# Optimization experiments

Hardware: AMD Instinct MI355X
Metric: run time of the kernel (lower is better)

## Reference

```python
import jax, jax.numpy as jnp
import numpy as np

TEMPERATURE = 0.5
EPS = 1e-8  # matches torch CosineSimilarity eps


def setup_inputs() -> dict:
    key = jax.random.key(0)
    k1, k2 = jax.random.split(key)
    N, D = 4096, 256
    z1 = jax.random.normal(k1, (N, D), dtype=jnp.float32)
    z2 = jax.random.normal(k2, (N, D), dtype=jnp.float32)
    return {"z1": z1, "z2": z2}


def reference(z1, z2):
    N = z1.shape[0]
    z = jnp.concatenate([z1, z2], axis=0)            # [2N, D]
    norm = jnp.linalg.norm(z, axis=-1, keepdims=True)
    zn = z / jnp.maximum(norm, EPS)                  # L2-normalized
    sim = (zn @ zn.T) / TEMPERATURE                  # [2N, 2N] cosine sim / temp
    # mask self-similarity on the diagonal
    diag = jnp.eye(2 * N, dtype=bool)
    sim = jnp.where(diag, -jnp.inf, sim)
    # positive pair labels: row i pairs with i+N (first half) or i-N (second half)
    labels = jnp.concatenate([jnp.arange(N) + N, jnp.arange(N)])
    logp = jax.nn.log_softmax(sim, axis=-1)
    loss = -jnp.mean(logp[jnp.arange(2 * N), labels])
    return loss
```

## Files before the change

kernel.cpp:

```cpp
#include <hip/hip_runtime.h>
#include <hip/hip_bf16.h>


#define NROWS 8192
#define NHALF 4096
#define DDIM  256

typedef __bf16 bf16;
typedef __bf16 bf16x4 __attribute__((ext_vector_type(4)));
typedef __bf16 bf16x8 __attribute__((ext_vector_type(8)));
typedef float  f32x4  __attribute__((ext_vector_type(4)));

__constant__ const float kTwoLog2e = 2.8853900817779268f;
__constant__ const float kLn2      = 0.6931471805599453f;

__device__ __forceinline__ const float* zrow(const float* z1, const float* z2, int r) {
  return (r < NHALF) ? (z1 + (size_t)r * DDIM) : (z2 + (size_t)(r - NHALF) * DDIM);
}

__global__ void k_normalize(const float* __restrict__ z1, const float* __restrict__ z2,
                            bf16* __restrict__ zn, float* __restrict__ invn,
                            float* __restrict__ rowsum, float* __restrict__ out) {
  const int wave = threadIdx.x >> 6, lane = threadIdx.x & 63;
  const int row = blockIdx.x * 4 + wave;
  const float* src = zrow(z1, z2, row);
  f32x4 v = *(const f32x4*)(src + lane * 4);
  float ss = v.x * v.x + v.y * v.y + v.z * v.z + v.w * v.w;
#pragma unroll
  for (int off = 1; off < 64; off <<= 1) ss += __shfl_xor(ss, off);
  const float inv = 1.0f / fmaxf(sqrtf(ss), 1e-8f);
  bf16x4 o;
  o.x = (bf16)(v.x * inv); o.y = (bf16)(v.y * inv);
  o.z = (bf16)(v.z * inv); o.w = (bf16)(v.w * inv);
  *(bf16x4*)(zn + (size_t)row * DDIM + lane * 4) = o;
  if (lane == 0) { invn[row] = inv; rowsum[row] = 0.0f; }
  if (blockIdx.x == 0 && threadIdx.x == 0) out[0] = 0.0f;
}

#define NBLK 512

typedef const __attribute__((address_space(1))) unsigned int* as1_u32p;
typedef __attribute__((address_space(3))) unsigned int* as3_u32p;

__device__ __forceinline__ void load_lds16(const void* g, void* l) {
  __builtin_amdgcn_global_lo\
ad_lds((as1_u32p)g, (as3_u32p)l, 16, 0, 0);
}

__global__ __launch_bounds__(256, 2) void k_gram(const bf16* __restrict__ zn,
                                                 float* __restrict__ rowsum) {
  __shared__ __align__(16) unsigned char ldsb[2][64 * 512];
  const int tid  = threadIdx.x;
  const int wave = tid >> 6, lane = tid & 63;
  const int quad = lane >> 4, l15 = lane & 15;

  const int I      = blockIdx.x >> 3;
  const int chunk  = blockIdx.x & 7;
  const int base_d = chunk * 4;
  const int n      = (chunk == 7 && I < 32) ? 10 : 8;
  const int R0     = I * 128 + wave * 32;

  auto cbase = [&](int t) -> int {
    const int d = base_d + (t >> 1);
    const int J = (I + d) & 63;
    return J * 128 + (t & 1) * 64;
  };
  auto issue_dma = [&](int t, int b) {
    const unsigned char* s = (const unsigned char*)(zn + (size_t)cbase(t) * DDIM);
#pragma unroll
    for (int j = 0; j < 8; ++j) {
      const int p = (wave * 8 + j) * 64 + lane;
      const int r = p >> 5;
      const int q = (p & 31) ^ (r & 15);
      load_lds16(s + r * 512 + q * 16, &ldsb[b][(wave * 8 + j) * 1024]);
    }
  };

  issue_dma(0, 0);
  __builtin_amdgcn_sched_barrier(0);

  bf16x8 a[2][8];
#pragma unroll
  for (int s = 0; s < 2; ++s) {
    const bf16x8* ap = (const bf16x8*)(zn + (size_t)(R0 + s * 16 + l15) * DDIM);
#pragma unroll
    for (int kk = 0; kk < 8; ++kk) a[s][kk] = ap[kk * 4 + quad];
  }
  __builtin_amdgcn_sched_barrier(0);

  issue_dma(1, 1);
  __builtin_amdgcn_sched_barrier(0);

  float sum[2][4] = {{0.f, 0.f, 0.f, 0.f}, {0.f, 0.f, 0.f, 0.f}};
  const f32x4 zero4 = {0.f, 0.f, 0.f, 0.f};

  for (int t = 0; t < n; ++t) {
    if (t == n - 1) asm volatile("s_waitcnt vmcnt(0)" ::: "memory");
    else            asm volatile("s_waitcnt vmcnt(8)" ::: "memory");
    __builtin_amdgcn_s_barrier();
    __builtin_amdgcn_sched_barrier(0);

    const unsigned char* bp = ldsb[t & 1];

    f32x4 acc[2][4];
#pragma unroll
    for (int s = 0; s < 2; ++s)
#pragma unroll
      for (int cs = 0; cs < 4; ++cs) acc[s][cs] = zero4;

    __builtin_amdgcn_s_setprio(1);
#pragma unroll
    for (int kk = 0; kk < 8; ++kk) {
      bf16x8 b[4];
#pragma unroll
      for (int cs = 0; cs < 4; ++cs) {
        const int rb = cs * 16 + l15;
        const int sl = (kk * 4 + quad) ^ (rb & 15);
        b[cs] = *(const bf16x8*)(bp + rb * 512 + sl * 16);
      }
#pragma unroll
      for (int s = 0; s < 2; ++s)
#pragma unroll
        for (int cs = 0; cs < 4; ++cs)
          acc[s][cs] =
              __builtin_amdgcn_mfma_f32_16x16x32_bf16(a[s][kk], b[cs], acc[s][cs], 0, 0, 0);
    }
    __builtin_amdgcn_s_setprio(0);

    const bool dg = (chunk == 0 && t < 2);
    const int cb = cbase(t);
#pragma unroll
    for (int cs = 0; cs < 4; ++cs) {
      float c = 0.f;
#pragma unroll
      for (int s = 0; s < 2; ++s)
#pragma unroll
        for (int r = 0; r < 4; ++r) {
          const float e = __builtin_amdgcn_exp2f(acc[s][cs][r] * kTwoLog2e);
          sum[s][r] += e;
          c += e;
        }
      if (!dg) {
        c += __shfl_xor(c, 16); c += __shfl_xor(c, 32);
        if (quad == 0) atomicAdd(&rowsum[cb + cs * 16 + l15], c);
      }
    }

    __builtin_amdgcn_s_barrier();
    __builtin_amdgcn_sched_barrier(0);
    if (t + 2 < n) {
      issue_dma(t + 2, t & 1);
      __builtin_amdgcn_sched_barrier(0);
    }
  }

#pragma unroll
  for (int s = 0; s < 2; ++s)
#pragma unroll
    for (int r = 0; r < 4; ++r) {
      float v = sum[s][r];
      v += __shfl_xor(v, 1); v += __shfl_xor(v, 2);
      v += __shfl_xor(v, 4); v += __shfl_xor(v, 8);
      if (l15 == 0) atomicAdd(&rowsum[R0 + s * 16 + quad * 4 + r], v);
    }
}

__global__ void k_finalize(const float* __restrict__ z1, const float* __restrict__ z2,
                           const bf16* __restrict__ zn, const float* __restrict__ invn,
                           const float* __restrict__ rowsum, float* __restrict__ out) {
  const int wave = threadIdx.x >> 6, lane = threadIdx.x & 63;
  const int row = blockIdx.x * 4 + wave;
  const int pr = (row < NHALF) ? row + NHALF : row - NHALF;

  f32x4 a4 = *(const f32x4*)(zrow(z1, z2, row) + lane * 4);
  f32x4 b4 = *(const f32x4*)(zrow(z1, z2, pr) + lane * 4);
  bf16x4 nb = *(const bf16x4*)(zn + (size_t)row * DDIM + lane * 4);

  float pd = a4.x * b4.x + a4.y * b4.y + a4.z * b4.z + a4.w * b4.w;
  float f0 = (float)nb.x, f1 = (float)nb.y, f2 = (float)nb.z, f3 = (float)nb.w;
  float nd = f0 * f0 + f1 * f1 + f2 * f2 + f3 * f3;
#pragma unroll
  for (int off = 1; off < 64; off <<= 1) {
    pd += __shfl_xor(pd, off);
    nd += __shfl_xor(nd, off);
  }
  __shared__ float wsum[4];
  if (lane == 0) {
    const float p = 2.0f * pd * invn[row] * invn[pr];
    const float dexp = __builtin_amdgcn_exp2f(kTwoLog2e * nd);
    const float lse = __builtin_amdgcn_logf(rowsum[row] - dexp) * kLn2;
    wsum[wave] = lse - p;
  }
  __syncthreads();
  if (threadIdx.x == 0)
    atomicAdd(out, (wsum[0] + wsum[1] + wsum[2] + wsum[3]) * (1.0f / (float)NROWS));
}

extern "C" void kernel_launch(void* const* d_in, const int* in_sizes, int n_in,
                              void* d_out, int out_size, void* d_ws, size_t ws_size,
                              hipStream_t stream) {
  const float* z1 = (const float*)d_in[0];
  const float* z2 = (const float*)d_in[1];
  unsigned char* ws = (unsigned char*)d_ws;

  bf16* zn = (bf16*)ws;
  float* invn = (float*)(ws + (size_t)NROWS * DDIM * sizeof(bf16));
  float* rowsum = invn + NROWS;
  float* out = (float*)d_out;

  hipLaunchKernelGGL(k_normalize, dim3(NROWS / 4), dim3(256), 0, stream, z1, z2, zn, invn, rowsum,
                     out);
  hipLaunchKernelGGL(k_gram, dim3(NBLK), dim3(256), 0, stream, zn, rowsum);
  hipLaunchKernelGGL(k_finalize, dim3(NROWS / 4), dim3(256), 0, stream, z1, z2, zn, invn, rowsum,
                     out);
}
```

Baseline: 117.0 us.

## Fuse normalize, gram and finalize into one cooperative kernel with grid syncs

Merges the three kernels into a single cooperative launch of 512 blocks that uses grid-wide syncs between the normalize, gram and finalize phases, with each block handling 16 rows in the per-row phases. This removes two kernel launch boundaries and their drain/ramp gaps. The cost is two grid barriers, lower parallelism in the normalize and finalize phases, and dependence on co-residency of all 512 blocks. If the cooperative launch fails, it falls back to the original three launches.

Result: slower. 218.2 us (+86.4%).

```diff
diff --git a/kernel.cpp b/kernel.cpp
--- a/kernel.cpp
+++ b/kernel.cpp
@@ -1,10 +1,14 @@
 #include <hip/hip_runtime.h>
 #include <hip/hip_bf16.h>
+#include <hip/hip_cooperative_groups.h>
+
+namespace cg = cooperative_groups;
 
 
 #define NROWS 8192
 #define NHALF 4096
 #define DDIM  256
+#define NBLK  512
 
 typedef __bf16 bf16;
 typedef __bf16 bf16x4 __attribute__((ext_vector_type(4)));
@@ -18,44 +22,41 @@
   return (r < NHALF) ? (z1 + (size_t)r * DDIM) : (z2 + (size_t)(r - NHALF) * DDIM);
 }
 
-__global__ void k_normalize(const float* __restrict__ z1, const float* __restrict__ z2,
-                            bf16* __restrict__ zn, float* __restrict__ invn,
-                            float* __restrict__ rowsum, float* __restrict__ out) {
-  const int wave = threadIdx.x >> 6, lane = threadIdx.x & 63;
-  const int row = blockIdx.x * 4 + wave;
-  const float* src = zrow(z1, z2, row);
-  f32x4 v = *(const f32x4*)(src + lane * 4);
-  float ss = v.x * v.x + v.y * v.y + v.z * v.z + v.w * v.w;
-#pragma unroll
-  for (int off = 1; off < 64; off <<= 1) ss += __shfl_xor(ss, off);
-  const float inv = 1.0f / fmaxf(sqrtf(ss), 1e-8f);
-  bf16x4 o;
-  o.x = (bf16)(v.x * inv); o.y = (bf16)(v.y * inv);
-  o.z = (bf16)(v.z * inv); o.w = (bf16)(v.w * inv);
-  *(bf16x4*)(zn + (size_t)row * DDIM + lane * 4) = o;
-  if (lane == 0) { invn[row] = inv; rowsum[row] = 0.0f; }
-  if (blockIdx.x == 0 && threadIdx.x == 0) out[0] = 0.0f;
-}
-
-#define NBLK 512
-
 typedef const __attribute__((address_space(1))) unsigned int* as1_u32p;
 typedef __attribute__((address_space(3))) unsigned int* as3_u32p;
 
 __device__ __forceinline__ void load_lds16(const void* g, void* l) {
-  __builtin_amdgcn_global_lo\
-ad_lds((as1_u32p)g, (as3_u32p)l, 16, 0, 0);
-}
-
-__global__ __launch_bounds__(256, 2) void k_gram(const bf16* __restrict__ zn,
-                                                 float* __restrict__ rowsum) {
-  __shared__ __align__(16) unsigned char ldsb[2][64 * 512];
+  __builtin_amdgcn_global_load_lds((as1_u32p)g, (as3_u32p)l, 16, 0, 0);
+}
+
+
+__device__ __forceinline__ void normalize_rows(int row0, int nrows_per, const float* z1,
+                                               const float* z2, bf16* zn, float* invn,
+                                               float* rowsum) {
+  const int wave = threadIdx.x >> 6, lane = threadIdx.x & 63;
+  for (int i = 0; i < nrows_per; ++i) {
+    const int row = row0 + wave * nrows_per + i;
+    f32x4 v = *(const f32x4*)(zrow(z1, z2, row) + lane * 4);
+    float ss = v.x * v.x + v.y * v.y + v.z * v.z + v.w * v.w;
+#pragma unroll
+    for (int off = 1; off < 64; off <<= 1) ss += __shfl_xor(ss, off);
+    const float inv = 1.0f / fmaxf(sqrtf(ss), 1e-8f);
+    bf16x4 o;
+    o.x = (bf16)(v.x * inv); o.y = (bf16)(v.y * inv);
+    o.z = (bf16)(v.z * inv); o.w = (bf16)(v.w * inv);
+    *(bf16x4*)(zn + (size_t)row * DDIM + lane * 4) = o;
+    if (lane == 0) { invn[row] = inv; rowsum[row] = 0.0f; }
+  }
+}
+
+__device__ __forceinline__ void gram_body(unsigned char (*ldsb)[64 * 512], const bf16* zn,
+                                          float* rowsum, int bid) {
   const int tid  = threadIdx.x;
   const int wave = tid >> 6, lane = tid & 63;
   const int quad = lane >> 4, l15 = lane & 15;
 
-  const int I      = blockIdx.x >> 3;
-  const int chunk  = blockIdx.x & 7;
+  const int I      = bid >> 3;
+  const int chunk  = bid & 7;
   const int base_d = chunk * 4;
   const int n      = (chunk == 7 && I < 32) ? 10 : 8;
   const int R0     = I * 128 + wave * 32;
@@ -165,32 +166,80 @@
     }
 }
 
+__device__ __forceinline__ float finalize_rows(int row0, int nrows_per, const float* z1,
+                                               const float* z2, const bf16* zn,
+                                               const float* invn, const float* rowsum) {
+  const int wave = threadIdx.x >> 6, lane = threadIdx.x & 63;
+  float cacc = 0.0f;
+  for (int i = 0; i < nrows_per; ++i) {
+    const int row = row0 + wave * nrows_per + i;
+    const int pr = (row < NHALF) ? row + NHALF : row - NHALF;
+    f32x4 a4 = *(const f32x4*)(zrow(z1, z2, row) + lane * 4);
+    f32x4 b4 = *(const f32x4*)(zrow(z1, z2, pr) + lane * 4);
+    bf16x4 nb = *(const bf16x4*)(zn + (size_t)row * DDIM + lane * 4);
+    float pd = a4.x * b4.x + a4.y * b4.y + a4.z * b4.z + a4.w * b4.w;
+    float f0 = (float)nb.x, f1 = (float)nb.y, f2 = (float)nb.z, f3 = (float)nb.w;
+    float nd = f0 * f0 + f1 * f1 + f2 * f2 + f3 * f3;
+#pragma unroll
+    for (int off = 1; off < 64; off <<= 1) {
+      pd += __shfl_xor(pd, off);
+      nd += __shfl_xor(nd, off);
+    }
+    const float p = 2.0f * pd * invn[row] * invn[pr];
+    const float dexp = __builtin_amdgcn_exp2f(kTwoLog2e * nd);
+    const float lse = __builtin_amdgcn_logf(rowsum[row] - dexp) * kLn2;
+    cacc += lse - p;
+  }
+  return cacc;
+}
+
+__global__ __launch_bounds__(256, 2) void k_fused(const float* __restrict__ z1,
+                                                  const float* __restrict__ z2,
+                                                  bf16* __restrict__ zn,
+                                                  float* __restrict__ invn,
+                                                  float* __restrict__ rowsum,
+                                                  float* __restrict__ out) {
+  __shared__ __align__(16) unsigned char ldsb[2][64 * 512];
+  const int tid = threadIdx.x;
+
+  normalize_rows(blockIdx.x * 16, 4, z1, z2, zn, invn, rowsum);
+  if (blockIdx.x == 0 && tid == 0) out[0] = 0.0f;
+
+  cg::this_grid().sync();
+
+  gram_body(ldsb, zn, rowsum, blockIdx.x);
+
+  cg::this_grid().sync();
+
+  const float cacc = finalize_rows(blockIdx.x * 16, 4, z1, z2, zn, invn, rowsum);
+  float* wsum = (float*)&ldsb[0][0];
+  const int wave = tid >> 6, lane = tid & 63;
+  if (lane == 0) wsum[wave] = cacc;
+  __syncthreads();
+  if (tid == 0)
+    atomicAdd(out, (wsum[0] + wsum[1] + wsum[2] + wsum[3]) * (1.0f / (float)NROWS));
+}
+
+__global__ void k_normalize(const float* __restrict__ z1, const float* __restrict__ z2,
+                            bf16* __restrict__ zn, float* __restrict__ invn,
+                            float* __restrict__ rowsum, float* __restrict__ out) {
+  normalize_rows(blockIdx.x * 4, 1, z1, z2, zn, invn, rowsum);
+  if (blockIdx.x == 0 && threadIdx.x == 0) out[0] = 0.0f;
+}
+
+__global__ __launch_bounds__(256, 2) void k_gram(const bf16* __restrict__ zn,
+                                                 float* __restrict__ rowsum) {
+  __shared__ __align__(16) unsigned char ldsb[2][64 * 512];
+  gram_body(ldsb, zn, rowsum, blockIdx.x);
+}
+
 __global__ void k_finalize(const float* __restrict__ z1, const float* __restrict__ z2,
                            const bf16* __restrict__ zn, const float* __restrict__ invn,
                            const float* __restrict__ rowsum, float* __restrict__ out) {
+  const float cacc = finalize_rows(blockIdx.x * 4, 1, z1, z2, zn, invn, rowsum);
+  __shared__ float wsum[4];
   const int wave = threadIdx.x >> 6, lane = threadIdx.x & 63;
-  const int row = blockIdx.x * 4 + wave;
-  const int pr = (row < NHALF) ? row + NHALF : row - NHALF;
-
-  f32x4 a4 = *(const f32x4*)(zrow(z1, z2, row) + lane * 4);
-  f32x4 b4 = *(const f32x4*)(zrow(z1, z2, pr) + lane * 4);
-  bf16x4 nb = *(const bf16x4*)(zn + (size_t)row * DDIM + lane * 4);
-
-  float pd = a4.x * b4.x + a4.y * b4.y + a4.z * b4.z + a4.w * b4.w;
-  float f0 = (float)nb.x, f1 = (float)nb.y, f2 = (float)nb.z, f3 = (float)nb.w;
-  float nd = f0 * f0 + f1 * f1 + f2 * f2 + f3 * f3;
-#pragma unroll
-  for (int off = 1; off < 64; off <<= 1) {
-    pd += __shfl_xor(pd, off);
-    nd += __shfl_xor(nd, off);
-  }
-  __shared__ float wsum[4];
-  if (lane == 0) {
-    const float p = 2.0f * pd * invn[row] * invn[pr];
-    const float dexp = __builtin_amdgcn_exp2f(kTwoLog2e * nd);
-    const float lse = __builtin_amdgcn_logf(rowsum[row] - dexp) * kLn2;
-    wsum[wave] = lse - p;
-  }
+  if (lane == 0) wsum[wave] = cacc;
   __syncthreads();
   if (threadIdx.x == 0)
     atomicAdd(out, (wsum[0] + wsum[1] + wsum[2] + wsum[3]) * (1.0f / (float)NROWS));
@@ -208,9 +257,14 @@
   float* rowsum = invn + NROWS;
   float* out = (float*)d_out;
 
-  hipLaunchKernelGGL(k_normalize, dim3(NROWS / 4), dim3(256), 0, stream, z1, z2, zn, invn, rowsum,
-                     out);
-  hipLaunchKernelGGL(k_gram, dim3(NBLK), dim3(256), 0, stream, zn, rowsum);
-  hipLaunchKernelGGL(k_finalize, dim3(NROWS / 4), dim3(256), 0, stream, z1, z2, zn, invn, rowsum,
-                     out);
-}
+  void* args[] = {(void*)&z1, (void*)&z2, (void*)&zn, (void*)&invn, (void*)&rowsum, (void*)&out};
+  hipError_t err =
+      hipLaunchCooperativeKernel((const void*)k_fused, dim3(NBLK), dim3(256), args, 0, stream);
+  if (err != hipSuccess) {
+    hipLaunchKernelGGL(k_normalize, dim3(NROWS / 4), dim3(256), 0, stream, z1, z2, zn, invn,
+                       rowsum, out);
+    hipLaunchKernelGGL(k_gram, dim3(NBLK), dim3(256), 0, stream, zn, rowsum);
+    hipLaunchKernelGGL(k_finalize, dim3(NROWS / 4), dim3(256), 0, stream, z1, z2, zn, invn,
+                       rowsum, out);
+  }
+}
```
